# Kernel tuning notes

Hardware: AMD Instinct MI355X
Metric: run time of the kernel (lower is better)

## Reference

```python
import jax, jax.numpy as jnp
import numpy as np

FILTER_K = 100  # filter_K from __init__
NUM_CLASSES = 1000


def setup_inputs() -> dict:
    key = jax.random.key(0)
    ks = jax.random.split(key, 7)
    B, Din, D, C, N = 256, 2048, 512, NUM_CLASSES, 50000
    x = jax.random.normal(ks[0], (B, Din), jnp.float32)
    Wf = jax.random.normal(ks[1], (Din, D), jnp.float32) * 0.02
    Wc = jax.random.normal(ks[2], (C, D), jnp.float32) * 0.05
    bc = jax.random.normal(ks[3], (C,), jnp.float32) * 0.01
    supports_in = jax.random.normal(ks[4], (N, D), jnp.float32)
    ent_in = jax.random.uniform(ks[5], (N,), jnp.float32)
    labels_idx = jax.random.randint(ks[6], (N,), 0, C)
    return {"x": x, "Wf": Wf, "Wc": Wc, "bc": bc,
            "supports_in": supports_in, "ent_in": ent_in, "labels_idx": labels_idx}


def _softmax_entropy(logits):
    # -(softmax * log_softmax).sum(1), computed stably in one pass
    logp = jax.nn.log_softmax(logits, axis=1)
    return -(jnp.exp(logp) * logp).sum(axis=1)


def reference(x, Wf, Wc, bc, supports_in, ent_in, labels_idx):
    C = Wc.shape[0]
    z = x @ Wf                    # featurizer: [B, D]
    p = z @ Wc.T + bc             # classifier logits: [B, C]
    yhat = jax.nn.one_hot(jnp.argmax(p, axis=1), C, dtype=z.dtype)
    ent_new = _softmax_entropy(p)
    labels_in = jax.nn.one_hot(labels_idx, C, dtype=z.dtype)

    # grow support memory
    supports = jnp.concatenate([supports_in, z], axis=0)   # [M, D]
    labels = jnp.concatenate([labels_in, yhat], axis=0)    # [M, C]
    ent = jnp.concatenate([ent_in, ent_new], axis=0)       # [M]

    # select_supports: per-class keep FILTER_K lowest-entropy entries.
    # Torch gathers a variable-size subset; equivalent fixed-shape form is a
    # boolean mask (non-selected rows contribute zero to the weights matmul).
    y = jnp.argmax(labels, axis=1)
    M = ent.shape[0]
    order = jnp.lexsort((ent, y))            # sort by class, then entropy
    y_sorted = y[order]
    # rank of each entry within its class segment
    rank = jnp.arange(M) - jnp.searchsorted(y_sorted, y_sorted, side='left')
    mask = jnp.zeros((M,), bool).at[order].set(rank < FILTER_K)
    maskf = mask.astype(z.dtype)

    # normalize supports row-wise (F.normalize, eps=1e-12), then masked matmul
    s_norm = supports / jnp.maximum(
        jnp.linalg.norm(supports, axis=1, keepdims=True), 1e-12)
    weights = (s_norm * maskf[:, None]).T @ (labels * maskf[:, None])  # [D, C]
    weights = weights / jnp.maximum(
        jnp.linalg.norm(weights, axis=0, keepdims=True), 1e-12)
    return z @ weights            # [B, C]
```

## Files before the change

### kernel.cpp

```cpp
#include <hip/hip_runtime.h>
#include <math.h>

#define BB   256
#define DIN  2048
#define DD   512
#define CC   1000
#define NN   50000
#define FILTER_K 100
#define SLOT 512
#define CSTRIDE 16

#define SK1  32
#define SKP  8
#define NBLK 512
#define NGRP 8
#define GSZ  (NBLK / NGRP)

#define Z_OFF     0
#define CNT_OFF   (Z_OFF + BB*DD)
#define BAR_BASE  16384
#define ARR_IDX(g)   (BAR_BASE + (g)*1024)
#define GFLG_IDX(g)  (BAR_BASE + (8+(g))*1024)
#define GLBC_IDX     (BAR_BASE + 16*1024)
#define GLBF_IDX     (BAR_BASE + 17*1024)
#define CNT_INTS  (16384 + 20*1024)
#define EI_OFF    (CNT_OFF + CNT_INTS)
#define WN_OFF    (EI_OFF + CC*SLOT*2)
#define ZP_OFF    (WN_OFF + CC*DD)
#define PP_OFF    (ZP_OFF + SK1*BB*DD)

#define SMEM_F 3712

typedef float f32x4 __attribute__((ext_vector_type(4)));
typedef float f32x2 __attribute__((ext_vector_type(2)));

__device__ __forceinline__ void st_wc4(float* p, float4 v) {
  f32x4 w = {v.x, v.y, v.z, v.w};
  asm volatile("global_store_dwordx4 %0, %1, off sc0 sc1" :: "v"(p), "v"(w) : "memory");
}
__device__ __forceinline__ void st_wc2(float* p, float a, float b) {
  f32x2 w = {a, b};
  asm volatile("global_store_dwordx2 %0, %1, off sc0 sc1" :: "v"(p), "v"(w) : "memory");
}
__device__ __forceinline__ void st_wc1(float* p, float a) {
  asm volatile("global_store_dword %0, %1, off sc0 sc1" :: "v"(p), "v"(a) : "memory");
}
__device__ __forceinline__ float2 ld_cv2(const float2* p) {
  unsigned long long r = __hip_atomic_load((const unsigned long long*)p,
      __ATOMIC_RELAXED, __HIP_MEMORY_SCOPE_AGENT);
  float2 o;
  o.x = __uint_as_float((unsigned)(r & 0xffffffffULL));
  o.y = __uint_as_float((unsigned)(r >> 32));
  return o;
}
__device__ __forceinline__ int ld_ci(const int* p) {
  return __hip_atomic_load(p, __ATOMIC_RELAXED, __HIP_MEMORY_SCOPE_AGENT);
}

__device__ __forceinline__ void gsync(int* cnt, int epoch, int grp, bool leader) {
  asm volatile("s_waitcnt vmcnt(0) lgkmcnt(0)" ::: "memory");
  __syncthreads();
  if (threadIdx.x == 0) {
    int t = __hip_atomic_fetch_add(&cnt[ARR_IDX(grp)], 1, __ATOMIC_RELAXED,
                                   __HIP_MEMORY_SCOPE_AGENT);
    if (t == epoch * GSZ - 1) {
      int u = __hip_atomic_fetch_add(&cnt[GLBC_IDX], 1, __ATOMIC_RELAXED,
                                     __HIP_MEMORY_SCOPE_AGENT);
      if (u == epoch * NGRP - 1)
        __hip_atomic_store(&cnt[GLBF_IDX], epoch, __ATOMIC_RELAXED,
                           __HIP_MEMORY_SCOPE_AGENT);
    }
    if (leader) {
      while (__hip_atomic_load(&cnt[GLBF_IDX], __ATOMIC_RELAXED,
                               __HIP_MEMORY_SCOPE_AGENT) < epoch)
        __builtin_amdgcn_s_sleep(4);
      __hip_atomic_store(&cnt[GFLG_IDX(grp)], epoch, __ATOMIC_RELAXED,
                         __HIP_MEMORY_SCOPE_AGENT);
    } else {
      while (__hip_atomic_load(&cnt[GFLG_IDX(grp)], __ATOMIC_RELAXED,
                               __HIP_MEMORY_SCOPE_AGENT) < epoch)
        __builtin_amdgcn_s_sleep(8);
    }
  }
  __syncthreads();
}

__device__ __forceinline__ void do_class(
    int c, int tid, float* smem, const float* supports_in, const float* z,
    const float2* ei, const int* cnt, float* wn) {
  int*   sel = (int*)smem;
  float* se  = smem + SLOT;
  int*   si  = (int*)(smem + 2*SLOT);
  float (*part)[DD] = (float(*)[DD])(smem + 3*SLOT);
  float* tot = smem + 3*SLOT + 4*DD;
  const int lane = tid & 63, wid = tid >> 6;
  int n = ld_ci(&cnt[c * CSTRIDE]); if (n > SLOT) n = SLOT;

  int seln;
  if (n <= FILTER_K) {
    seln = n;
    for (int i = tid; i < n; i += 256)
      sel[i] = __float_as_int(ld_cv2(&ei[(size_t)c * SLOT + i]).y);
  } else {
    for (int i = tid; i < SLOT; i += 256) {
      if (i < n) {
        float2 pr = ld_cv2(&ei[(size_t)c * SLOT + i]);
        se[i] = pr.x; si[i] = __float_as_int(pr.y);
      } else { se[i] = INFINITY; si[i] = 0x7fffffff; }
    }
    __syncthreads();
    for (int k = 2; k <= SLOT; k <<= 1)
      for (int j = k >> 1; j > 0; j >>= 1) {
        for (int i = tid; i < SLOT; i += 256) {
          int ixj = i ^ j;
          if (ixj > i) {
            bool up = ((i & k) == 0);
            float e1 = se[i], e2 = se[ixj];
            int i1 = si[i], i2 = si[ixj];
            bool gt = (e1 > e2) || (e1 == e2 && i1 > i2);
            if (gt == up) { se[i] = e2; se[ixj] = e1; si[i] = i2; si[ixj] = i1; }
          }
        }
        __syncthreads();
      }
    seln = FILTER_K;
    for (int i = tid; i < FILTER_K; i += 256) sel[i] = si[i];
  }
  __syncthreads();
  const int seln_pad = (seln + 15) & ~15;
  if (seln > 0)
    for (int i = seln + tid; i < seln_pad; i += 256) sel[i] = sel[0];
  __syncthreads();

  float4 a0 = make_float4(0.f, 0.f, 0.f, 0.f), a1 = a0;
  for (int t = wid * 4; t < seln_pad; t += 16) {
    float4 u0[4], u1[4]; float s[4];
#pragma unroll
    for (int j = 0; j < 4; ++j) {
      int r = sel[t + j];
      const float4* p4 = (const float4*)((r < NN)
          ? supports_in + (size_t)r * DD : z + (size_t)(r - NN) * DD);
      u0[j] = p4[lane * 2]; u1[j] = p4[lane * 2 + 1];
    }
#pragma unroll
    for (int j = 0; j < 4; ++j)
      s[j] = u0[j].x * u0[j].x + u0[j].y * u0[j].y + u0[j].z * u0[j].z
           + u0[j].w * u0[j].w + u1[j].x * u1[j].x + u1[j].y * u1[j].y
           + u1[j].z * u1[j].z + u1[j].w * u1[j].w;
#pragma unroll
    for (int o = 1; o < 64; o <<= 1) {
#pragma unroll
      for (int j = 0; j < 4; ++j) s[j] += __shfl_xor(s[j], o, 64);
    }
#pragma unroll
    for (int j = 0; j < 4; ++j) {
      float sc = (t + j < seln) ? 1.0f / fmaxf(sqrtf(s[j]), 1e-12f) : 0.f;
      a0.x += u0[j].x * sc; a0.y += u0[j].y * sc;
      a0.z += u0[j].z * sc; a0.w += u0[j].w * sc;
      a1.x += u1[j].x * sc; a1.y += u1[j].y * sc;
      a1.z += u1[j].z * sc; a1.w += u1[j].w * sc;
    }
  }

  *(float4*)&part[wid][lane * 8] = a0;
  *(float4*)&part[wid][lane * 8 + 4] = a1;
  __syncthreads();
  const int d = tid * 2;
  float wx = part[0][d] + part[1][d] + part[2][d] + part[3][d];
  float wy = part[0][d + 1] + part[1][d + 1] + part[2][d + 1] + part[3][d + 1];
  float ss = wx * wx + wy * wy;
#pragma unroll
  for (int o = 1; o < 64; o <<= 1) ss += __shfl_xor(ss, o, 64);
  if (lane == 0) tot[wid] = ss;
  __syncthreads();
  float S = tot[0] + tot[1] + tot[2] + tot[3];
  float sc = 1.0f / fmaxf(sqrtf(S), 1e-12f);
  st_wc2(wn + (size_t)c * DD + 2 * tid, wx * sc, wy * sc);
}

__device__ __forceinline__ void gemm_abt_tile(
    const float* __restrict__ A, const float* __restrict__ Bm,
    float* __restrict__ Cb, float* smem, int tid, int m0, int n0, int k0) {
  float (*As)[68] = (float(*)[68])smem;
  float (*Bs)[68] = (float(*)[68])(smem + 16 * 68);
  const int ar = tid >> 2, ac = (tid & 3) * 4;
  const int tm = (tid >> 4) * 4, tn = (tid & 15) * 4;
  float acc[4][4] = {};
  float4 av = *(const float4*)&A[(size_t)(m0 + ar) * DD + k0 + ac];
  float4 bv = make_float4(0.f, 0.f, 0.f, 0.f);
  if (n0 + ar < CC) bv = *(const float4*)&Bm[(size_t)(n0 + ar) * DD + k0 + ac];
  for (int kk = 0; kk < 64; kk += 16) {
    __syncthreads();
    As[ac + 0][ar] = av.x; As[ac + 1][ar] = av.y;
    As[ac + 2][ar] = av.z; As[ac + 3][ar] = av.w;
    Bs[ac + 0][ar] = bv.x; Bs[ac + 1][ar] = bv.y;
    Bs[ac + 2][ar] = bv.z; Bs[ac + 3][ar] = bv.w;
    __syncthreads();
    if (kk + 16 < 64) {
      av = *(const float4*)&A[(size_t)(m0 + ar) * DD + k0 + kk + 16 + ac];
      if (n0 + ar < CC)
        bv = *(const float4*)&Bm[(size_t)(n0 + ar) * DD + k0 + kk + 16 + ac];
    }
#pragma unroll
    for (int q = 0; q < 16; ++q) {
      float4 a = *(const float4*)&As[q][tm];
      float4 b = *(const float4*)&Bs[q][tn];
      float aa[4] = {a.x, a.y, a.z, a.w};
      float bb[4] = {b.x, b.y, b.z, b.w};
#pragma unroll
      for (int i = 0; i < 4; ++i)
#pragma unroll
        for (int j = 0; j < 4; ++j) acc[i][j] += aa[i] * bb[j];
    }
  }
#pragma unroll
  for (int i = 0; i < 4; ++i) {
    int n = n0 + tn;
    if (n + 3 < CC) {
      st_wc4(&Cb[(size_t)(m0 + tm + i) * CC + n],
             make_float4(acc[i][0], acc[i][1], acc[i][2], acc[i][3]));
    } else {
#pragma unroll
      for (int j = 0; j < 4; ++j)
        if (n + j < CC) st_wc1(&Cb[(size_t)(m0 + tm + i) * CC + n + j], acc[i][j]);
    }
  }
}

__global__ __launch_bounds__(256, 2) void megaA(
    const float* x, const float* Wf, const float* Wc, const float* bc,
    const float* ent_in, const int* labels_idx, float* ws) {
  __shared__ __align__(16) float smem[SMEM_F];
  float*  z     = ws + Z_OFF;
  int*    cnt   = (int*)(ws + CNT_OFF);
  float2* ei    = (float2*)(ws + EI_OFF);
  float*  zpart = ws + ZP_OFF;
  float*  ppart = ws + PP_OFF;
  const int bid = blockIdx.x, tid = threadIdx.x;
  const int grp = bid >> 6;
  const bool leader = (bid & 63) == 0;

  {
    float (*As)[68]  = (float(*)[68])smem;
    float (*Bs)[132] = (float(*)[132])(smem + 16 * 68);
    const int m0 = ((bid >> 2) & 3) * 64;
    const int n0 = (bid & 3) * 128;
    const int k0 = (bid >> 4) * 64;
    const int ar = tid >> 2, ac = (tid & 3) * 4;
    const int br = tid >> 4, bcn = (tid & 15) * 8;
    const int tm = (tid >> 4) * 4, tn = (tid & 15) * 4;
    float acc[4][8] = {};
    float4 av  = *(const float4*)&x[(size_t)(m0 + ar) * DIN + k0 + ac];
    float4 bv0 = *(const float4*)&Wf[(size_t)(k0 + br) * DD + n0 + bcn];
    float4 bv1 = *(const float4*)&Wf[(size_t)(k0 + br) * DD + n0 + bcn + 4];
    for (int kk = 0; kk < 64; kk += 16) {
      __syncthreads();
      As[ac + 0][ar] = av.x; As[ac + 1][ar] = av.y;
      As[ac + 2][ar] = av.z; As[ac + 3][ar] = av.w;
      *(float4*)&Bs[br][bcn] = bv0;
      *(float4*)&Bs[br][bcn + 4] = bv1;
      __syncthreads();
      if (kk + 16 < 64) {
        av  = *(const float4*)&x[(size_t)(m0 + ar) * DIN + k0 + kk + 16 + ac];
        bv0 = *(const float4*)&Wf[(size_t)(k0 + kk + 16 + br) * DD + n0 + bcn];
        bv1 = *(const float4*)&Wf[(size_t)(k0 + kk + 16 + br) * DD + n0 + bcn + 4];
      }
#pragma unroll
      for (int q = 0; q < 16; ++q) {
        float4 a  = *(const float4*)&As[q][tm];
        float4 b0 = *(const float4*)&Bs[q][tn];
        float4 b1 = *(const float4*)&Bs[q][tn + 64];
        float aa[4] = {a.x, a.y, a.z, a.w};
        float bb[8] = {b0.x, b0.y, b0.z, b0.w, b1.x, b1.y, b1.z, b1.w};
#pragma unroll
        for (int i = 0; i < 4; ++i)
#pragma unroll
          for (int j = 0; j < 8; ++j) acc[i][j] += aa[i] * bb[j];
      }
    }
    float* Cb = zpart + (size_t)(bid >> 4) * BB * DD;
#pragma unroll
    for (int i = 0; i < 4; ++i) {
      st_wc4(&Cb[(size_t)(m0 + tm + i) * DD + n0 + tn],
             make_float4(acc[i][0], acc[i][1], acc[i][2], acc[i][3]));
      st_wc4(&Cb[(size_t)(m0 + tm + i) * DD + n0 + 64 + tn],
             make_float4(acc[i][4], acc[i][5], acc[i][6], acc[i][7]));
    }
  }
  gsync(cnt, 1, grp, leader);

  if (bid < 128) {
    const int n4 = BB * DD / 4;
    int i = bid * 256 + tid;
    if (i < n4) {
      const float4* p4 = (const float4*)zpart;
      float4 a = p4[i];
#pragma unroll
      for (int s = 1; s < SK1; ++s) {
        float4 b = p4[(size_t)s * n4 + i];
        a.x += b.x; a.y += b.y; a.z += b.z; a.w += b.w;
      }
      st_wc4(z + 4 * (size_t)i, a);
    }
  } else if (bid < 324) {
    int m = (bid - 128) * 256 + tid;
    if (m < NN) {
      int c = labels_idx[m];
      int pos = atomicAdd(&cnt[c * CSTRIDE], 1);
      if (pos < SLOT) {
        st_wc2((float*)&ei[(size_t)c * SLOT + pos], ent_in[m], __int_as_float(m));
      }
    }
  }
  gsync(cnt, 2, grp, leader);

  {
    const int ks = bid >> 6;
    gemm_abt_tile(z, Wc, ppart + (size_t)ks * BB * CC, smem, tid,
                  ((bid >> 4) & 3) * 64, (bid & 15) * 64, ks * 64);
  }
  gsync(cnt, 3, grp, leader);

  if (bid < BB) {
    float* smv = smem; int* smi = (int*)(smem + 4);
    float* ssm = smem + 8; float* tsm = smem + 12;
    const int b = bid;
    const int lane = tid & 63, wid = tid >> 6;
    const int cbase = tid * 4;
    float rr[4];
    float mv = -INFINITY; int mi = 0x7fffffff;
    if (cbase < CC) {
      float4 v = *(const float4*)&bc[cbase];
#pragma unroll
      for (int s = 0; s < SKP; ++s) {
        float4 pv = *(const float4*)&ppart[(size_t)s * BB * CC + (size_t)b * CC + cbase];
        v.x += pv.x; v.y += pv.y; v.z += pv.z; v.w += pv.w;
      }
      rr[0] = v.x; rr[1] = v.y; rr[2] = v.z; rr[3] = v.w;
#pragma unroll
      for (int j = 0; j < 4; ++j)
        if (rr[j] > mv) { mv = rr[j]; mi = cbase + j; }
    } else { rr[0] = rr[1] = rr[2] = rr[3] = -INFINITY; }
#pragma unroll
    for (int o = 32; o > 0; o >>= 1) {
      float ov = __shfl_down(mv, o, 64);
      int oi = __shfl_down(mi, o, 64);
      if (ov > mv || (ov == mv && oi < mi)) { mv = ov; mi = oi; }
    }
    if (lane == 0) { smv[wid] = mv; smi[wid] = mi; }
    __syncthreads();
    if (tid == 0) {
#pragma unroll
      for (int w = 1; w < 4; ++w)
        if (smv[w] > smv[0] || (smv[w] == smv[0] && smi[w] < smi[0])) {
          smv[0] = smv[w]; smi[0] = smi[w];
        }
    }
    __syncthreads();
    const float m = smv[0]; const int am = smi[0];
    float s = 0.f, t = 0.f;
    if (cbase < CC) {
#pragma unroll
      for (int j = 0; j < 4; ++j) {
        float u = rr[j] - m;
        float e = expf(u);
        s += e; t += u * e;
      }
    }
#pragma unroll
    for (int o = 32; o > 0; o >>= 1) {
      s += __shfl_down(s, o, 64);
      t += __shfl_down(t, o, 64);
    }
    if (lane == 0) { ssm[wid] = s; tsm[wid] = t; }
    __syncthreads();
    if (tid == 0) {
      float S = ssm[0] + ssm[1] + ssm[2] + ssm[3];
      float T = tsm[0] + tsm[1] + tsm[2] + tsm[3];
      float ent = logf(S) - T / S;
      int pos = atomicAdd(&cnt[am * CSTRIDE], 1);
      if (pos < SLOT) {
        st_wc2((float*)&ei[(size_t)am * SLOT + pos], ent, __int_as_float(NN + b));
      }
    }
  }
}

__global__ __launch_bounds__(256, 4) void megaB1(
    const float* supports_in, float* ws) {
  __shared__ __align__(16) float smem[SMEM_F];
  float*  z   = ws + Z_OFF;
  int*    cnt = (int*)(ws + CNT_OFF);
  float2* ei  = (float2*)(ws + EI_OFF);
  float*  wn  = ws + WN_OFF;
  do_class(blockIdx.x, threadIdx.x, smem, supports_in, z, ei, cnt, wn);
}

__global__ __launch_bounds__(256, 2) void megaB2(
    float* out, float* ws) {
  __shared__ __align__(16) float smem[16 * 20 + 16 * 68];
  float* z  = ws + Z_OFF;
  float* wn = ws + WN_OFF;
  const int bid = blockIdx.x, tid = threadIdx.x;
  float (*As)[20] = (float(*)[20])smem;
  float (*Bs)[68] = (float(*)[68])(smem + 16 * 20);
  const int m0 = (bid >> 4) * 16;
  const int n0 = (bid & 15) * 64;
  const int arow = tid >> 4, ak = tid & 15;
  const int br = tid >> 2, bcl = (tid & 3) * 4;
  const int tr = tid >> 4, tn4 = (tid & 15) * 4;
  float acc[4] = {};
  float av = z[(size_t)(m0 + arow) * DD + ak];
  float4 bv = make_float4(0.f, 0.f, 0.f, 0.f);
  if (n0 + br < CC) bv = *(const float4*)&wn[(size_t)(n0 + br) * DD + bcl];
  for (int k0 = 0; k0 < DD; k0 += 16) {
    __syncthreads();
    As[ak][arow] = av;
    Bs[bcl + 0][br] = bv.x; Bs[bcl + 1][br] = bv.y;
    Bs[bcl + 2][br] = bv.z; Bs[bcl + 3][br] = bv.w;
    __syncthreads();
    if (k0 + 16 < DD) {
      av = z[(size_t)(m0 + arow) * DD + k0 + 16 + ak];
      if (n0 + br < CC)
        bv = *(const float4*)&wn[(size_t)(n0 + br) * DD + k0 + 16 + bcl];
    }
#pragma unroll
    for (int q = 0; q < 16; ++q) {
      float a = As[q][tr];
      float4 b = *(const float4*)&Bs[q][tn4];
      acc[0] += a * b.x; acc[1] += a * b.y;
      acc[2] += a * b.z; acc[3] += a * b.w;
    }
  }
  int n = n0 + tn4;
  if (n + 3 < CC) {
    *(float4*)&out[(size_t)(m0 + tr) * CC + n] =
        make_float4(acc[0], acc[1], acc[2], acc[3]);
  } else {
#pragma unroll
    for (int j = 0; j < 4; ++j)
      if (n + j < CC) out[(size_t)(m0 + tr) * CC + n + j] = acc[j];
  }
}

extern "C" void kernel_launch(void* const* d_in, const int* in_sizes, int n_in,
                              void* d_out, int out_size, void* d_ws, size_t ws_size,
                              hipStream_t stream) {
  (void)in_sizes; (void)n_in; (void)out_size; (void)ws_size;
  const float* x           = (const float*)d_in[0];
  const float* Wf          = (const float*)d_in[1];
  const float* Wc          = (const float*)d_in[2];
  const float* bc          = (const float*)d_in[3];
  const float* supports_in = (const float*)d_in[4];
  const float* ent_in      = (const float*)d_in[5];
  const int*   labels_idx  = (const int*)d_in[6];
  float* out = (float*)d_out;
  float* W = (float*)d_ws;
  int* cnt = (int*)(W + CNT_OFF);

  hipMemsetAsync(cnt, 0, CNT_INTS * sizeof(int), stream);
  hipLaunchKernelGGL(megaA, dim3(NBLK), dim3(256), 0, stream,
                     x, Wf, Wc, bc, ent_in, labels_idx, W);
  hipLaunchKernelGGL(megaB1, dim3(CC), dim3(256), 0, stream, supports_in, W);
  hipLaunchKernelGGL(megaB2, dim3(256), dim3(256), 0, stream, out, W);
}
```

Measured before the change: 223.3 us.

## Split final z@W GEMM into split-K partial tiles plus reduction kernel

The final output GEMM (256x512 by 512x1000) moves from 256 blocks of small 16x64 tiles to 512 blocks. These reuse the existing 64x64 gemm_abt_tile with an 8-way split over K, writing partial sums to a workspace region. A second small kernel then adds the 8 partials into the output. Separately, the per-class support gather now uses nontemporal vector loads and vector-typed accumulation. The split adds an extra launch and round-trips the partial sums through memory, in exchange for more parallelism and better tile reuse.

After: 212.7 us. 1.05x faster.

```diff
diff --git a/kernel.cpp b/kernel.cpp
--- a/kernel.cpp
+++ b/kernel.cpp
@@ -12,6 +12,7 @@
 
 #define SK1  32
 #define SKP  8
+#define SKO  8
 #define NBLK 512
 #define NGRP 8
 #define GSZ  (NBLK / NGRP)
@@ -28,6 +29,7 @@
 #define WN_OFF    (EI_OFF + CC*SLOT*2)
 #define ZP_OFF    (WN_OFF + CC*DD)
 #define PP_OFF    (ZP_OFF + SK1*BB*DD)
+#define OP_OFF    (PP_OFF + SKP*BB*CC)
 
 #define SMEM_F 3712
 
@@ -132,21 +134,22 @@
     for (int i = seln + tid; i < seln_pad; i += 256) sel[i] = sel[0];
   __syncthreads();
 
-  float4 a0 = make_float4(0.f, 0.f, 0.f, 0.f), a1 = a0;
+  f32x4 a0 = {0.f, 0.f, 0.f, 0.f}, a1 = {0.f, 0.f, 0.f, 0.f};
   for (int t = wid * 4; t < seln_pad; t += 16) {
-    float4 u0[4], u1[4]; float s[4];
+    f32x4 u0[4], u1[4]; float s[4];
 #pragma unroll
     for (int j = 0; j < 4; ++j) {
       int r = sel[t + j];
-      const float4* p4 = (const float4*)((r < NN)
+      const f32x4* p4 = (const f32x4*)((r < NN)
           ? supports_in + (size_t)r * DD : z + (size_t)(r - NN) * DD);
-      u0[j] = p4[lane * 2]; u1[j] = p4[lane * 2 + 1];
+      u0[j] = __builtin_nontemporal_load(p4 + lane * 2);
+      u1[j] = __builtin_nontemporal_load(p4 + lane * 2 + 1);
     }
 #pragma unroll
     for (int j = 0; j < 4; ++j)
-      s[j] = u0[j].x * u0[j].x + u0[j].y * u0[j].y + u0[j].z * u0[j].z
-           + u0[j].w * u0[j].w + u1[j].x * u1[j].x + u1[j].y * u1[j].y
-           + u1[j].z * u1[j].z + u1[j].w * u1[j].w;
+      s[j] = u0[j][0] * u0[j][0] + u0[j][1] * u0[j][1] + u0[j][2] * u0[j][2]
+           + u0[j][3] * u0[j][3] + u1[j][0] * u1[j][0] + u1[j][1] * u1[j][1]
+           + u1[j][2] * u1[j][2] + u1[j][3] * u1[j][3];
 #pragma unroll
     for (int o = 1; o < 64; o <<= 1) {
 #pragma unroll
@@ -155,15 +158,13 @@
 #pragma unroll
     for (int j = 0; j < 4; ++j) {
       float sc = (t + j < seln) ? 1.0f / fmaxf(sqrtf(s[j]), 1e-12f) : 0.f;
-      a0.x += u0[j].x * sc; a0.y += u0[j].y * sc;
-      a0.z += u0[j].z * sc; a0.w += u0[j].w * sc;
-      a1.x += u1[j].x * sc; a1.y += u1[j].y * sc;
-      a1.z += u1[j].z * sc; a1.w += u1[j].w * sc;
-    }
-  }
-
-  *(float4*)&part[wid][lane * 8] = a0;
-  *(float4*)&part[wid][lane * 8 + 4] = a1;
+      a0 += u0[j] * sc;
+      a1 += u1[j] * sc;
+    }
+  }
+
+  *(f32x4*)&part[wid][lane * 8] = a0;
+  *(f32x4*)&part[wid][lane * 8 + 4] = a1;
   __syncthreads();
   const int d = tid * 2;
   float wx = part[0][d] + part[1][d] + part[2][d] + part[3][d];
@@ -396,50 +397,29 @@
   do_class(blockIdx.x, threadIdx.x, smem, supports_in, z, ei, cnt, wn);
 }
 
-__global__ __launch_bounds__(256, 2) void megaB2(
-    float* out, float* ws) {
-  __shared__ __align__(16) float smem[16 * 20 + 16 * 68];
-  float* z  = ws + Z_OFF;
-  float* wn = ws + WN_OFF;
+__global__ __launch_bounds__(256, 2) void megaB2a(float* ws) {
+  __shared__ __align__(16) float smem[2 * 16 * 68];
+  float* z     = ws + Z_OFF;
+  float* wn    = ws + WN_OFF;
+  float* opart = ws + OP_OFF;
   const int bid = blockIdx.x, tid = threadIdx.x;
-  float (*As)[20] = (float(*)[20])smem;
-  float (*Bs)[68] = (float(*)[68])(smem + 16 * 20);
-  const int m0 = (bid >> 4) * 16;
-  const int n0 = (bid & 15) * 64;
-  const int arow = tid >> 4, ak = tid & 15;
-  const int br = tid >> 2, bcl = (tid & 3) * 4;
-  const int tr = tid >> 4, tn4 = (tid & 15) * 4;
-  float acc[4] = {};
-  float av = z[(size_t)(m0 + arow) * DD + ak];
-  float4 bv = make_float4(0.f, 0.f, 0.f, 0.f);
-  if (n0 + br < CC) bv = *(const float4*)&wn[(size_t)(n0 + br) * DD + bcl];
-  for (int k0 = 0; k0 < DD; k0 += 16) {
-    __syncthreads();
-    As[ak][arow] = av;
-    Bs[bcl + 0][br] = bv.x; Bs[bcl + 1][br] = bv.y;
-    Bs[bcl + 2][br] = bv.z; Bs[bcl + 3][br] = bv.w;
-    __syncthreads();
-    if (k0 + 16 < DD) {
-      av = z[(size_t)(m0 + arow) * DD + k0 + 16 + ak];
-      if (n0 + br < CC)
-        bv = *(const float4*)&wn[(size_t)(n0 + br) * DD + k0 + 16 + bcl];
-    }
-#pragma unroll
-    for (int q = 0; q < 16; ++q) {
-      float a = As[q][tr];
-      float4 b = *(const float4*)&Bs[q][tn4];
-      acc[0] += a * b.x; acc[1] += a * b.y;
-      acc[2] += a * b.z; acc[3] += a * b.w;
-    }
-  }
-  int n = n0 + tn4;
-  if (n + 3 < CC) {
-    *(float4*)&out[(size_t)(m0 + tr) * CC + n] =
-        make_float4(acc[0], acc[1], acc[2], acc[3]);
-  } else {
-#pragma unroll
-    for (int j = 0; j < 4; ++j)
-      if (n + j < CC) out[(size_t)(m0 + tr) * CC + n + j] = acc[j];
+  const int ks = bid >> 6;
+  gemm_abt_tile(z, wn, opart + (size_t)ks * BB * CC, smem, tid,
+                ((bid >> 4) & 3) * 64, (bid & 15) * 64, ks * 64);
+}
+
+__global__ __launch_bounds__(256) void megaB2b(float* out, float* ws) {
+  float* opart = ws + OP_OFF;
+  const int bid = blockIdx.x, tid = threadIdx.x;
+  const int cbase = tid * 4;
+  if (cbase < CC) {
+    float4 a = *(const float4*)&opart[(size_t)bid * CC + cbase];
+#pragma unroll
+    for (int s = 1; s < SKO; ++s) {
+      float4 b = *(const float4*)&opart[(size_t)s * BB * CC + (size_t)bid * CC + cbase];
+      a.x += b.x; a.y += b.y; a.z += b.z; a.w += b.w;
+    }
+    *(float4*)&out[(size_t)bid * CC + cbase] = a;
   }
 }
 
@@ -462,5 +442,6 @@
   hipLaunchKernelGGL(megaA, dim3(NBLK), dim3(256), 0, stream,
                      x, Wf, Wc, bc, ent_in, labels_idx, W);
   hipLaunchKernelGGL(megaB1, dim3(CC), dim3(256), 0, stream, supports_in, W);
-  hipLaunchKernelGGL(megaB2, dim3(256), dim3(256), 0, stream, out, W);
-}
+  hipLaunchKernelGGL(megaB2a, dim3(NBLK), dim3(256), 0, stream, W);
+  hipLaunchKernelGGL(megaB2b, dim3(256), dim3(256), 0, stream, out, W);
+}
```
